# Kernel tuning notes

Measured on AMD Instinct MI355X. Metric: run time of the kernel, lower is better.

## Reference

```python
import jax, jax.numpy as jnp
import numpy as np

N_NODES = 100000


def _gcn_conv(x, W, b, src, dst, num_nodes):
    """PyG-style GCNConv: out = D^{-1/2}(A+I)D^{-1/2} (x W) + b.
    src/dst already include self-loops. Degree over dst with unit edge weights."""
    h = x @ W  # [N, F_out]
    ones = jnp.ones(dst.shape, dtype=h.dtype)
    deg = jax.ops.segment_sum(ones, dst, num_segments=num_nodes)  # [N]
    dinv = jnp.where(deg > 0, jax.lax.rsqrt(deg), 0.0)
    norm = dinv[src] * dinv[dst]  # [E]
    msgs = norm[:, None] * h[src]  # [E, F_out] gather
    agg = jax.ops.segment_sum(msgs, dst, num_segments=num_nodes)  # scatter-add
    return agg + b


def setup_inputs() -> dict:
    key = jax.random.key(0)
    ks = jax.random.split(key, 8)
    N, E = N_NODES, 1600000
    F_in, H, F_out = 128, 128, 64
    x = jax.random.normal(ks[0], (N, F_in), dtype=jnp.float32)
    edge_index = jax.random.randint(ks[1], (2, E), 0, N, dtype=jnp.int32)
    s_in = 1.0 / np.sqrt(F_in)
    s_h = 1.0 / np.sqrt(H)
    s_o = 1.0 / np.sqrt(F_out)
    W1 = jax.random.uniform(ks[2], (F_in, H), jnp.float32, -s_in, s_in)
    b1 = jnp.zeros((H,), jnp.float32)
    W2 = jax.random.uniform(ks[3], (H, F_out), jnp.float32, -s_h, s_h)
    b2 = jnp.zeros((F_out,), jnp.float32)
    Wout = jax.random.uniform(ks[4], (F_out, 1), jnp.float32, -s_o, s_o)
    bout = jax.random.uniform(ks[5], (1,), jnp.float32, -s_o, s_o)
    return {"x": x, "edge_index": edge_index, "W1": W1, "b1": b1,
            "W2": W2, "b2": b2, "Wout": Wout, "bout": bout}


def reference(x, edge_index, W1, b1, W2, b2, Wout, bout):
    N = x.shape[0]
    loops = jnp.arange(N, dtype=edge_index.dtype)
    src = jnp.concatenate([edge_index[0], loops])  # add self-loops
    dst = jnp.concatenate([edge_index[1], loops])
    h = jax.nn.relu(_gcn_conv(x, W1, b1, src, dst, N))
    h = jax.nn.relu(_gcn_conv(h, W2, b2, src, dst, N))
    return h @ Wout + bout  # [N, 1]
```

## Files before the change

kernel.cpp:

```cpp
#include <hip/hip_runtime.h>
#include <math.h>

#define NN 100000
#define CAP 64

typedef _Float16 hv2 __attribute__((ext_vector_type(2)));
typedef _Float16 hv4 __attribute__((ext_vector_type(4)));


__global__ __launch_bounds__(256) void k_fillg(const int* __restrict__ src,
                                               const int* __restrict__ dst,
                                               int* __restrict__ cursor,
                                               int* __restrict__ csr, int E, int NBF,
                                               const float* __restrict__ x,
                                               const float* __restrict__ W,
                                               _Float16* __restrict__ hs, int M) {
    __shared__ float xt[64][132];
    int bid = blockIdx.x;
    int tid = threadIdx.x;
    if (bid & 1) {
        int fid = bid >> 1;
        if (fid >= NBF) return;
        int e0 = fid * 1024 + tid;
        int dd[4], ss[4], pp[4];
        bool ok[4];
        #pragma unroll
        for (int k = 0; k < 4; ++k) {
            int e = e0 + k * 256;
            ok[k] = (e < E);
            dd[k] = ok[k] ? dst[e] : 0;
            ss[k] = ok[k] ? src[e] : 0;
        }
        #pragma unroll
        for (int k = 0; k < 4; ++k)
            if (ok[k]) pp[k] = atomicAdd(&cursor[dd[k]], 1);
        #pragma unroll
        for (int k = 0; k < 4; ++k)
            if (ok[k] && pp[k] < CAP)
                __builtin_nontemporal_store(ss[k], &csr[(size_t)dd[k] * CAP + pp[k]]);
        return;
    }
    int gid = bid >> 1;
    int row0 = gid * 64;
    if (row0 >= M) return;
    #pragma unroll
    for (int it = 0; it < 8; ++it) {
        int idx = it * 256 + tid;
        int r = idx >> 5;
        int c4 = (idx & 31) << 2;
        float4 v = make_float4(0.f, 0.f, 0.f, 0.f);
        if (row0 + r < M) v = *(const float4*)&x[(size_t)(row0 + r) * 128 + c4];
        *(float4*)&xt[r][c4] = v;
    }
    __syncthreads();
    int ct = tid & 31, rt = tid >> 5;
    int c0 = ct * 4, r0 = rt * 8;
    float acc[8][4];
    #pragma unroll
    for (int i = 0; i < 8; ++i)
        #pragma unroll
        for (int j = 0; j < 4; ++j) acc[i][j] = 0.f;

    for (int k = 0; k < 128; k += 4) {
        float4 w0 = *(const float4*)&W[(size_t)(k + 0) * 128 + c0];
        float4 w1 = *(const float4*)&W[(size_t)(k + 1) * 128 + c0];
        float4 w2 = *(const float4*)&W[(size_t)(k + 2) * 128 + c0];
        float4 w3 = *(const float4*)&W[(size_t)(k + 3) * 128 + c0];
        #pragma unroll
        for (int i = 0; i < 8; ++i) {
            float4 xv = *(const float4*)&xt[r0 + i][k];
            acc[i][0] += xv.x * w0.x + xv.y * w1.x + xv.z * w2.x + xv.w * w3.x;
            acc[i][1] += xv.x * w0.y + xv.y * w1.y + xv.z * w2.y + xv.w * w3.y;
            acc[i][2] += xv.x * w0.z + xv.y * w1.z + xv.z * w2.z + xv.w * w3.z;
            acc[i][3] += xv.x * w0.w + xv.y * w1.w + xv.z * w2.w + xv.w * w3.w;
        }
    }
    #pragma unroll
    for (int i = 0; i < 8; ++i) {
        int r = row0 + r0 + i;
        if (r < M) {
            hv4 o;
            o.x = (_Float16)acc[i][0];
            o.y = (_Float16)acc[i][1];
            o.z = (_Float16)acc[i][2];
            o.w = (_Float16)acc[i][3];
            *(hv4*)&hs[(size_t)r * 128 + c0] = o;
        }
    }
}


__global__ void k_deg(const int* __restrict__ cursor, float* __restrict__ dinv, int n) {
    int i = blockIdx.x * 256 + threadIdx.x;
    if (i < n) dinv[i] = rsqrtf((float)(cursor[i] + 1));
}


__global__ __launch_bounds__(256) void k_agg1(const _Float16* __restrict__ hs,
                                              const int* __restrict__ csr,
                                              const int* __restrict__ cursor,
                                              const float* __restrict__ dinv,
                                              const float* __restrict__ b,
                                              _Float16* __restrict__ out, int n) {
    int wave = (blockIdx.x * 256 + threadIdx.x) >> 6;
    int lane = threadIdx.x & 63;
    if (wave >= n) return;
    int node = wave;
    int start = node * CAP;
    int cnt = __builtin_amdgcn_readfirstlane(cursor[node]);
    cnt = cnt < CAP ? cnt : CAP;
    int h = lane >> 5;
    int f0 = 4 * (lane & 31);

    int my_idx = (lane < cnt) ? csr[start + lane] : 0;
    float my_dinv = (lane < cnt) ? dinv[my_idx] : 0.f;

    float a0[4] = {0.f, 0.f, 0.f, 0.f};
    float a1r[4] = {0.f, 0.f, 0.f, 0.f};

    int j = 0;
    for (; j + 16 <= cnt; j += 16) {
        hv4 v[8];
        float ds[8];
        #pragma unroll
        for (int u = 0; u < 8; ++u) {
            int s = __shfl(my_idx, j + 2 * u + h, 64);
            ds[u] = __shfl(my_dinv, j + 2 * u + h, 64);
            v[u] = *(const hv4*)(hs + (size_t)s * 128 + f0);
        }
        #pragma unroll
        for (int u = 0; u < 8; ++u) {
            float* a = (u & 1) ? a1r : a0;
            a[0] += ds[u] * (float)v[u].x; a[1] += ds[u] * (float)v[u].y;
            a[2] += ds[u] * (float)v[u].z; a[3] += ds[u] * (float)v[u].w;
        }
    }
    for (; j + 2 <= cnt; j += 2) {
        int s = __shfl(my_idx, j + h, 64);
        float ds = __shfl(my_dinv, j + h, 64);
        hv4 v = *(const hv4*)(hs + (size_t)s * 128 + f0);
        a0[0] += ds * (float)v.x; a0[1] += ds * (float)v.y;
        a0[2] += ds * (float)v.z; a0[3] += ds * (float)v.w;
    }
    if (j < cnt) {
        int s = __shfl(my_idx, j, 64);
        float ds = __shfl(my_dinv, j, 64);
        if (h == 0) {
            hv4 v = *(const hv4*)(hs + (size_t)s * 128 + f0);
            a0[0] += ds * (float)v.x; a0[1] += ds * (float)v.y;
            a0[2] += ds * (float)v.z; a0[3] += ds * (float)v.w;
        }
    }
    float dn = dinv[node];
    if (h == 0) {
        hv4 v = *(const hv4*)(hs + (size_t)node * 128 + f0);
        a0[0] += dn * (float)v.x; a0[1] += dn * (float)v.y;
        a0[2] += dn * (float)v.z; a0[3] += dn * (float)v.w;
    }

    float tot[4];
    #pragma unroll
    for (int i = 0; i < 4; ++i) {
        tot[i] = a0[i] + a1r[i];
        tot[i] += __shfl_xor(tot[i], 32, 64);
    }
    float4 bb = *(const float4*)&b[f0];
    hv4 o;
    o.x = (_Float16)fmaxf(dn * tot[0] + bb.x, 0.f);
    o.y = (_Float16)fmaxf(dn * tot[1] + bb.y, 0.f);
    o.z = (_Float16)fmaxf(dn * tot[2] + bb.z, 0.f);
    o.w = (_Float16)fmaxf(dn * tot[3] + bb.w, 0.f);
    if (h == 0)
        __builtin_nontemporal_store(o, (hv4*)&out[(size_t)node * 128 + f0]);
}


__global__ __launch_bounds__(256) void k_gemm2(const _Float16* __restrict__ a,
                                               const float* __restrict__ W,
                                               const float* __restrict__ dinv,
                                               _Float16* __restrict__ hs, int M) {
    __shared__ float xt[64][132];
    int tid = threadIdx.x;
    int row0 = blockIdx.x * 64;
    #pragma unroll
    for (int it = 0; it < 8; ++it) {
        int idx = it * 256 + tid;
        int r = idx >> 5;
        int c4 = (idx & 31) << 2;
        float4 v = make_float4(0.f, 0.f, 0.f, 0.f);
        if (row0 + r < M) {
            hv4 hvv = *(const hv4*)&a[(size_t)(row0 + r) * 128 + c4];
            v = make_float4((float)hvv.x, (float)hvv.y, (float)hvv.z, (float)hvv.w);
        }
        *(float4*)&xt[r][c4] = v;
    }
    __syncthreads();
    int ct = tid & 15, rt = tid >> 4;
    int c0 = ct * 4, r0 = rt * 4;
    float acc[4][4];
    #pragma unroll
    for (int i = 0; i < 4; ++i)
        #pragma unroll
        for (int j = 0; j < 4; ++j) acc[i][j] = 0.f;

    for (int k = 0; k < 128; k += 4) {
        float4 w0 = *(const float4*)&W[(size_t)(k + 0) * 64 + c0];
        float4 w1 = *(const float4*)&W[(size_t)(k + 1) * 64 + c0];
        float4 w2 = *(const float4*)&W[(size_t)(k + 2) * 64 + c0];
        float4 w3 = *(const float4*)&W[(size_t)(k + 3) * 64 + c0];
        #pragma unroll
        for (int i = 0; i < 4; ++i) {
            float4 xv = *(const float4*)&xt[r0 + i][k];
            acc[i][0] += xv.x * w0.x + xv.y * w1.x + xv.z * w2.x + xv.w * w3.x;
            acc[i][1] += xv.x * w0.y + xv.y * w1.y + xv.z * w2.y + xv.w * w3.y;
            acc[i][2] += xv.x * w0.z + xv.y * w1.z + xv.z * w2.z + xv.w * w3.z;
            acc[i][3] += xv.x * w0.w + xv.y * w1.w + xv.z * w2.w + xv.w * w3.w;
        }
    }
    #pragma unroll
    for (int i = 0; i < 4; ++i) {
        int r = row0 + r0 + i;
        if (r < M) {
            float d = dinv[r];
            hv4 o;
            o.x = (_Float16)(acc[i][0] * d);
            o.y = (_Float16)(acc[i][1] * d);
            o.z = (_Float16)(acc[i][2] * d);
            o.w = (_Float16)(acc[i][3] * d);
            *(hv4*)&hs[(size_t)r * 64 + c0] = o;
        }
    }
}


__global__ __launch_bounds__(256) void k_agg2(const _Float16* __restrict__ hs,
                                              const int* __restrict__ csr,
                                              const int* __restrict__ cursor,
                                              const float* __restrict__ dinv,
                                              const float* __restrict__ b2,
                                              const float* __restrict__ Wout,
                                              const float* __restrict__ bout,
                                              float* __restrict__ out, int n) {
    int wave = (blockIdx.x * 256 + threadIdx.x) >> 6;
    int lane = threadIdx.x & 63;
    if (wave >= n) return;
    int node = wave;
    int start = node * CAP;
    int cnt = __builtin_amdgcn_readfirstlane(cursor[node]);
    cnt = cnt < CAP ? cnt : CAP;
    int q = lane >> 4;
    int f0 = 4 * (lane & 15);

    int my_idx = (lane < cnt) ? csr[start + lane] : 0;

    float a0[4] = {0.f, 0.f, 0.f, 0.f};
    float a1r[4] = {0.f, 0.f, 0.f, 0.f};

    int j = 0;
    for (; j + 16 <= cnt; j += 16) {
        hv4 v[4];
        #pragma unroll
        for (int u = 0; u < 4; ++u) {
            int s = __shfl(my_idx, j + 4 * u + q, 64);
            v[u] = *(const hv4*)(hs + (size_t)s * 64 + f0);
        }
        #pragma unroll
        for (int u = 0; u < 4; ++u) {
            float* a = (u & 1) ? a1r : a0;
            a[0] += (float)v[u].x; a[1] += (float)v[u].y;
            a[2] += (float)v[u].z; a[3] += (float)v[u].w;
        }
    }
    for (; j + 4 <= cnt; j += 4) {
        int s = __shfl(my_idx, j + q, 64);
        hv4 v = *(const hv4*)(hs + (size_t)s * 64 + f0);
        a0[0] += (float)v.x; a0[1] += (float)v.y;
        a0[2] += (float)v.z; a0[3] += (float)v.w;
    }
    int rem = cnt - j;
    if (rem > 0) {
        int s = __shfl(my_idx, j + (q < rem ? q : 0), 64);
        if (q < rem) {
            hv4 v = *(const hv4*)(hs + (size_t)s * 64 + f0);
            a0[0] += (float)v.x; a0[1] += (float)v.y;
            a0[2] += (float)v.z; a0[3] += (float)v.w;
        }
    }
    if (q == 0) {
        hv4 v = *(const hv4*)(hs + (size_t)node * 64 + f0);
        a0[0] += (float)v.x; a0[1] += (float)v.y;
        a0[2] += (float)v.z; a0[3] += (float)v.w;
    }

    float tot[4];
    #pragma unroll
    for (int i = 0; i < 4; ++i) {
        tot[i] = a0[i] + a1r[i];
        tot[i] += __shfl_xor(tot[i], 16, 64);
        tot[i] += __shfl_xor(tot[i], 32, 64);
    }
    float dn = dinv[node];
    float4 bb = *(const float4*)&b2[f0];
    float4 wv = *(const float4*)&Wout[f0];
    float p = fmaxf(dn * tot[0] + bb.x, 0.f) * wv.x
            + fmaxf(dn * tot[1] + bb.y, 0.f) * wv.y
            + fmaxf(dn * tot[2] + bb.z, 0.f) * wv.z
            + fmaxf(dn * tot[3] + bb.w, 0.f) * wv.w;
    p += __shfl_xor(p, 1, 64);
    p += __shfl_xor(p, 2, 64);
    p += __shfl_xor(p, 4, 64);
    p += __shfl_xor(p, 8, 64);
    if (lane == 0) __builtin_nontemporal_store(p + bout[0], &out[node]);
}


extern "C" void kernel_launch(void* const* d_in, const int* in_sizes, int n_in,
                              void* d_out, int out_size, void* d_ws, size_t ws_size,
                              hipStream_t stream) {
    const float* x    = (const float*)d_in[0];
    const int*   ei   = (const int*)d_in[1];
    const float* W1   = (const float*)d_in[2];
    const float* b1   = (const float*)d_in[3];
    const float* W2   = (const float*)d_in[4];
    const float* b2   = (const float*)d_in[5];
    const float* Wout = (const float*)d_in[6];
    const float* bout = (const float*)d_in[7];

    const int N = NN;
    const int E = in_sizes[1] / 2;
    const int* src = ei;
    const int* dst = ei + E;

    char* ws = (char*)d_ws;
    size_t off = 0;
    auto alloc = [&](size_t bytes) -> void* {
        void* p = ws + off;
        off = (off + bytes + 255) & ~(size_t)255;
        return p;
    };
    int*      cursor = (int*)alloc((size_t)N * 4);
    float*    dinv   = (float*)alloc((size_t)N * 4);
    int*      csr    = (int*)alloc((size_t)N * CAP * 4);
    _Float16* hs1    = (_Float16*)alloc((size_t)N * 128 * 2);
    _Float16* a1     = (_Float16*)alloc((size_t)N * 128 * 2);
    _Float16* hs2    = hs1;

    (void)hipMemsetAsync(cursor, 0, (size_t)N * 4, stream);

    int NBF = (E + 1023) / 1024;
    int NBG = (N + 63) / 64;
    int NB = NBF > NBG ? NBF : NBG;
    k_fillg<<<2 * NB, 256, 0, stream>>>(src, dst, cursor, csr, E, NBF, x, W1, hs1, N);
    k_deg  <<<(N + 255) / 256, 256, 0, stream>>>(cursor, dinv, N);
    k_agg1 <<<(N + 3) / 4, 256, 0, stream>>>(hs1, csr, cursor, dinv, b1, a1, N);
    k_gemm2<<<(N + 63) / 64, 256, 0, stream>>>(a1, W2, dinv, hs2, N);
    k_agg2 <<<(N + 3) / 4, 256, 0, stream>>>(hs2, csr, cursor, dinv, b2, Wout, bout,
                                             (float*)d_out, N);
}
```

Measured before the change: 261.8 us.

## Fuse layer-2 GEMM into aggregation and compute degree norms inline

Removes the degree kernel by computing rsqrt(deg+1) inline from the cursor counts. Reorders layer 2 to aggregate first on the 128-wide a1 features, then multiply by W2 per node. W2 is staged in LDS as fp16 and the GEMM, ReLU and output projection are fused into one kernel. This drops two launches and the hs2 round trip, but each gathered row is now 128 wide instead of 64, so gather traffic doubles. Every block also reloads W2 into LDS and runs a per-node matvec.

```diff
diff --git a/kernel.cpp b/kernel.cpp
--- a/kernel.cpp
+++ b/kernel.cpp
@@ -90,16 +90,9 @@
 }
 
 
-__global__ void k_deg(const int* __restrict__ cursor, float* __restrict__ dinv, int n) {
-    int i = blockIdx.x * 256 + threadIdx.x;
-    if (i < n) dinv[i] = rsqrtf((float)(cursor[i] + 1));
-}
-
-
 __global__ __launch_bounds__(256) void k_agg1(const _Float16* __restrict__ hs,
                                               const int* __restrict__ csr,
                                               const int* __restrict__ cursor,
-                                              const float* __restrict__ dinv,
                                               const float* __restrict__ b,
                                               _Float16* __restrict__ out, int n) {
     int wave = (blockIdx.x * 256 + threadIdx.x) >> 6;
@@ -107,13 +100,14 @@
     if (wave >= n) return;
     int node = wave;
     int start = node * CAP;
-    int cnt = __builtin_amdgcn_readfirstlane(cursor[node]);
-    cnt = cnt < CAP ? cnt : CAP;
+    int deg = __builtin_amdgcn_readfirstlane(cursor[node]);
+    int cnt = deg < CAP ? deg : CAP;
+    float dn = rsqrtf((float)(deg + 1));
     int h = lane >> 5;
     int f0 = 4 * (lane & 31);
 
     int my_idx = (lane < cnt) ? csr[start + lane] : 0;
-    float my_dinv = (lane < cnt) ? dinv[my_idx] : 0.f;
+    float my_dinv = (lane < cnt) ? rsqrtf((float)(cursor[my_idx] + 1)) : 0.f;
 
     float a0[4] = {0.f, 0.f, 0.f, 0.f};
     float a1r[4] = {0.f, 0.f, 0.f, 0.f};
@@ -151,7 +145,6 @@
             a0[2] += ds * (float)v.z; a0[3] += ds * (float)v.w;
         }
     }
-    float dn = dinv[node];
     if (h == 0) {
         hv4 v = *(const hv4*)(hs + (size_t)node * 128 + f0);
         a0[0] += dn * (float)v.x; a0[1] += dn * (float)v.y;
@@ -175,141 +168,109 @@
 }
 
 
-__global__ __launch_bounds__(256) void k_gemm2(const _Float16* __restrict__ a,
-                                               const float* __restrict__ W,
-                                               const float* __restrict__ dinv,
-                                               _Float16* __restrict__ hs, int M) {
-    __shared__ float xt[64][132];
+__global__ __launch_bounds__(256) void k_agg2f(const _Float16* __restrict__ a1,
+                                               const int* __restrict__ csr,
+                                               const int* __restrict__ cursor,
+                                               const float* __restrict__ W2,
+                                               const float* __restrict__ b2,
+                                               const float* __restrict__ Wout,
+                                               const float* __restrict__ bout,
+                                               float* __restrict__ out, int n) {
+    __shared__ _Float16 w2s[128 * 64];
+    __shared__ float gld[4][128];
     int tid = threadIdx.x;
-    int row0 = blockIdx.x * 64;
     #pragma unroll
     for (int it = 0; it < 8; ++it) {
-        int idx = it * 256 + tid;
-        int r = idx >> 5;
-        int c4 = (idx & 31) << 2;
-        float4 v = make_float4(0.f, 0.f, 0.f, 0.f);
-        if (row0 + r < M) {
-            hv4 hvv = *(const hv4*)&a[(size_t)(row0 + r) * 128 + c4];
-            v = make_float4((float)hvv.x, (float)hvv.y, (float)hvv.z, (float)hvv.w);
-        }
-        *(float4*)&xt[r][c4] = v;
+        int idx = it * 1024 + tid * 4;
+        float4 wv = *(const float4*)&W2[idx];
+        hv4 o;
+        o.x = (_Float16)wv.x; o.y = (_Float16)wv.y;
+        o.z = (_Float16)wv.z; o.w = (_Float16)wv.w;
+        *(hv4*)&w2s[idx] = o;
     }
     __syncthreads();
-    int ct = tid & 15, rt = tid >> 4;
-    int c0 = ct * 4, r0 = rt * 4;
-    float acc[4][4];
-    #pragma unroll
-    for (int i = 0; i < 4; ++i)
-        #pragma unroll
-        for (int j = 0; j < 4; ++j) acc[i][j] = 0.f;
-
-    for (int k = 0; k < 128; k += 4) {
-        float4 w0 = *(const float4*)&W[(size_t)(k + 0) * 64 + c0];
-        float4 w1 = *(const float4*)&W[(size_t)(k + 1) * 64 + c0];
-        float4 w2 = *(const float4*)&W[(size_t)(k + 2) * 64 + c0];
-        float4 w3 = *(const float4*)&W[(size_t)(k + 3) * 64 + c0];
-        #pragma unroll
-        for (int i = 0; i < 4; ++i) {
-            float4 xv = *(const float4*)&xt[r0 + i][k];
-            acc[i][0] += xv.x * w0.x + xv.y * w1.x + xv.z * w2.x + xv.w * w3.x;
-            acc[i][1] += xv.x * w0.y + xv.y * w1.y + xv.z * w2.y + xv.w * w3.y;
-            acc[i][2] += xv.x * w0.z + xv.y * w1.z + xv.z * w2.z + xv.w * w3.z;
-            acc[i][3] += xv.x * w0.w + xv.y * w1.w + xv.z * w2.w + xv.w * w3.w;
-        }
-    }
-    #pragma unroll
-    for (int i = 0; i < 4; ++i) {
-        int r = row0 + r0 + i;
-        if (r < M) {
-            float d = dinv[r];
-            hv4 o;
-            o.x = (_Float16)(acc[i][0] * d);
-            o.y = (_Float16)(acc[i][1] * d);
-            o.z = (_Float16)(acc[i][2] * d);
-            o.w = (_Float16)(acc[i][3] * d);
-            *(hv4*)&hs[(size_t)r * 64 + c0] = o;
-        }
-    }
-}
-
-
-__global__ __launch_bounds__(256) void k_agg2(const _Float16* __restrict__ hs,
-                                              const int* __restrict__ csr,
-                                              const int* __restrict__ cursor,
-                                              const float* __restrict__ dinv,
-                                              const float* __restrict__ b2,
-                                              const float* __restrict__ Wout,
-                                              const float* __restrict__ bout,
-                                              float* __restrict__ out, int n) {
-    int wave = (blockIdx.x * 256 + threadIdx.x) >> 6;
-    int lane = threadIdx.x & 63;
+
+    int w = tid >> 6, lane = tid & 63;
+    int wave = blockIdx.x * 4 + w;
     if (wave >= n) return;
     int node = wave;
     int start = node * CAP;
-    int cnt = __builtin_amdgcn_readfirstlane(cursor[node]);
-    cnt = cnt < CAP ? cnt : CAP;
-    int q = lane >> 4;
-    int f0 = 4 * (lane & 15);
+    int deg = __builtin_amdgcn_readfirstlane(cursor[node]);
+    int cnt = deg < CAP ? deg : CAP;
+    float dn = rsqrtf((float)(deg + 1));
+    int h = lane >> 5;
+    int f0 = 4 * (lane & 31);
 
     int my_idx = (lane < cnt) ? csr[start + lane] : 0;
+    float my_dinv = (lane < cnt) ? rsqrtf((float)(cursor[my_idx] + 1)) : 0.f;
 
     float a0[4] = {0.f, 0.f, 0.f, 0.f};
     float a1r[4] = {0.f, 0.f, 0.f, 0.f};
 
     int j = 0;
     for (; j + 16 <= cnt; j += 16) {
-        hv4 v[4];
-        #pragma unroll
-        for (int u = 0; u < 4; ++u) {
-            int s = __shfl(my_idx, j + 4 * u + q, 64);
-            v[u] = *(const hv4*)(hs + (size_t)s * 64 + f0);
-        }
-        #pragma unroll
-        for (int u = 0; u < 4; ++u) {
+        hv4 v[8];
+        float ds[8];
+        #pragma unroll
+        for (int u = 0; u < 8; ++u) {
+            int s = __shfl(my_idx, j + 2 * u + h, 64);
+            ds[u] = __shfl(my_dinv, j + 2 * u + h, 64);
+            v[u] = *(const hv4*)(a1 + (size_t)s * 128 + f0);
+        }
+        #pragma unroll
+        for (int u = 0; u < 8; ++u) {
             float* a = (u & 1) ? a1r : a0;
-            a[0] += (float)v[u].x; a[1] += (float)v[u].y;
-            a[2] += (float)v[u].z; a[3] += (float)v[u].w;
-        }
-    }
-    for (; j + 4 <= cnt; j += 4) {
-        int s = __shfl(my_idx, j + q, 64);
-        hv4 v = *(const hv4*)(hs + (size_t)s * 64 + f0);
-        a0[0] += (float)v.x; a0[1] += (float)v.y;
-        a0[2] += (float)v.z; a0[3] += (float)v.w;
-    }
-    int rem = cnt - j;
-    if (rem > 0) {
-        int s = __shfl(my_idx, j + (q < rem ? q : 0), 64);
-        if (q < rem) {
-            hv4 v = *(const hv4*)(hs + (size_t)s * 64 + f0);
-            a0[0] += (float)v.x; a0[1] += (float)v.y;
-            a0[2] += (float)v.z; a0[3] += (float)v.w;
-        }
-    }
-    if (q == 0) {
-        hv4 v = *(const hv4*)(hs + (size_t)node * 64 + f0);
-        a0[0] += (float)v.x; a0[1] += (float)v.y;
-        a0[2] += (float)v.z; a0[3] += (float)v.w;
+            a[0] += ds[u] * (float)v[u].x; a[1] += ds[u] * (float)v[u].y;
+            a[2] += ds[u] * (float)v[u].z; a[3] += ds[u] * (float)v[u].w;
+        }
+    }
+    for (; j + 2 <= cnt; j += 2) {
+        int s = __shfl(my_idx, j + h, 64);
+        float ds = __shfl(my_dinv, j + h, 64);
+        hv4 v = *(const hv4*)(a1 + (size_t)s * 128 + f0);
+        a0[0] += ds * (float)v.x; a0[1] += ds * (float)v.y;
+        a0[2] += ds * (float)v.z; a0[3] += ds * (float)v.w;
+    }
+    if (j < cnt) {
+        int s = __shfl(my_idx, j, 64);
+        float ds = __shfl(my_dinv, j, 64);
+        if (h == 0) {
+            hv4 v = *(const hv4*)(a1 + (size_t)s * 128 + f0);
+            a0[0] += ds * (float)v.x; a0[1] += ds * (float)v.y;
+            a0[2] += ds * (float)v.z; a0[3] += ds * (float)v.w;
+        }
+    }
+    if (h == 0) {
+        hv4 v = *(const hv4*)(a1 + (size_t)node * 128 + f0);
+        a0[0] += dn * (float)v.x; a0[1] += dn * (float)v.y;
+        a0[2] += dn * (float)v.z; a0[3] += dn * (float)v.w;
     }
 
     float tot[4];
     #pragma unroll
     for (int i = 0; i < 4; ++i) {
         tot[i] = a0[i] + a1r[i];
-        tot[i] += __shfl_xor(tot[i], 16, 64);
         tot[i] += __shfl_xor(tot[i], 32, 64);
     }
-    float dn = dinv[node];
-    float4 bb = *(const float4*)&b2[f0];
-    float4 wv = *(const float4*)&Wout[f0];
-    float p = fmaxf(dn * tot[0] + bb.x, 0.f) * wv.x
-            + fmaxf(dn * tot[1] + bb.y, 0.f) * wv.y
-            + fmaxf(dn * tot[2] + bb.z, 0.f) * wv.z
-            + fmaxf(dn * tot[3] + bb.w, 0.f) * wv.w;
+    if (h == 0) *(float4*)&gld[w][f0] = make_float4(tot[0], tot[1], tot[2], tot[3]);
+
+    float acc = 0.f;
+    const float* gw = gld[w];
+    #pragma unroll
+    for (int k = 0; k < 128; k += 4) {
+        float4 gv = *(const float4*)&gw[k];
+        acc += gv.x * (float)w2s[(k + 0) * 64 + lane];
+        acc += gv.y * (float)w2s[(k + 1) * 64 + lane];
+        acc += gv.z * (float)w2s[(k + 2) * 64 + lane];
+        acc += gv.w * (float)w2s[(k + 3) * 64 + lane];
+    }
+    float p = fmaxf(dn * acc + b2[lane], 0.f) * Wout[lane];
     p += __shfl_xor(p, 1, 64);
     p += __shfl_xor(p, 2, 64);
     p += __shfl_xor(p, 4, 64);
     p += __shfl_xor(p, 8, 64);
+    p += __shfl_xor(p, 16, 64);
+    p += __shfl_xor(p, 32, 64);
     if (lane == 0) __builtin_nontemporal_store(p + bout[0], &out[node]);
 }
 
@@ -339,11 +300,9 @@
         return p;
     };
     int*      cursor = (int*)alloc((size_t)N * 4);
-    float*    dinv   = (float*)alloc((size_t)N * 4);
     int*      csr    = (int*)alloc((size_t)N * CAP * 4);
     _Float16* hs1    = (_Float16*)alloc((size_t)N * 128 * 2);
     _Float16* a1     = (_Float16*)alloc((size_t)N * 128 * 2);
-    _Float16* hs2    = hs1;
 
     (void)hipMemsetAsync(cursor, 0, (size_t)N * 4, stream);
 
@@ -351,9 +310,7 @@
     int NBG = (N + 63) / 64;
     int NB = NBF > NBG ? NBF : NBG;
     k_fillg<<<2 * NB, 256, 0, stream>>>(src, dst, cursor, csr, E, NBF, x, W1, hs1, N);
-    k_deg  <<<(N + 255) / 256, 256, 0, stream>>>(cursor, dinv, N);
-    k_agg1 <<<(N + 3) / 4, 256, 0, stream>>>(hs1, csr, cursor, dinv, b1, a1, N);
-    k_gemm2<<<(N + 63) / 64, 256, 0, stream>>>(a1, W2, dinv, hs2, N);
-    k_agg2 <<<(N + 3) / 4, 256, 0, stream>>>(hs2, csr, cursor, dinv, b2, Wout, bout,
+    k_agg1 <<<(N + 3) / 4, 256, 0, stream>>>(hs1, csr, cursor, b1, a1, N);
+    k_agg2f<<<(N + 3) / 4, 256, 0, stream>>>(a1, csr, cursor, W2, b2, Wout, bout,
                                              (float*)d_out, N);
 }
```

New measurement: 300.7 us. +14.9%, slower.
